# Optimization experiments

Hardware: AMD Instinct MI355X
Metric: run time of the kernel (lower is better)

## Reference

```python
import jax, jax.numpy as jnp
import numpy as np

B, S, H = 1, 2048, 1024          # batch, seq, hidden_size
INTER, K, DST, DTR = 2048, 4, 16, 64  # intermediate, kernel, ssm_state, dt_rank


def setup_inputs() -> dict:
    key = jax.random.key(0)
    ks = jax.random.split(key, 10)
    sc = 0.02
    return {
        "x": jax.random.normal(ks[0], (B, S, H), jnp.float32),
        "W_in": jax.random.normal(ks[1], (H, 2 * INTER), jnp.float32) * sc,
        "conv_w": jax.random.normal(ks[2], (K, 1, INTER), jnp.float32) * sc,
        "conv_b": jax.random.normal(ks[3], (INTER,), jnp.float32) * sc,
        "W_x": jax.random.normal(ks[4], (INTER, DTR + 2 * DST), jnp.float32) * sc,
        "W_dt": jax.random.normal(ks[5], (DTR, INTER), jnp.float32) * sc,
        "b_dt": jax.random.normal(ks[6], (INTER,), jnp.float32) * sc,
        "A_log": jax.random.normal(ks[7], (INTER, DST), jnp.float32) * sc,
        "D": jax.random.normal(ks[8], (INTER,), jnp.float32) * sc,
        "W_out": jax.random.normal(ks[9], (INTER, H), jnp.float32) * sc,
    }


def _ssm(dA, dBu, C):
    # dA, dBu: (b, s, h, d); C: (b, s, d) -> y: (b, s, h)
    xs = (jnp.moveaxis(dA, 1, 0), jnp.moveaxis(dBu, 1, 0), jnp.moveaxis(C, 1, 0))
    state0 = jnp.zeros(dA.shape[:1] + dA.shape[2:], dA.dtype)  # (b, h, d)

    def step(state, inp):
        Ai, dBui, Ci = inp  # (b,h,d), (b,h,d), (b,d)
        state = Ai * state + dBui
        y = jnp.einsum('bhd,bd->bh', state, Ci)
        return state, y

    _, ys = jax.lax.scan(step, state0, xs)  # ys: (s, b, h)
    return jnp.moveaxis(ys, 0, 1)


def reference(x, W_in, conv_w, conv_b, W_x, W_dt, b_dt, A_log, D, W_out):
    proj = x @ W_in                              # (b, s, 2*inter)
    raw, gate = jnp.split(proj, 2, axis=-1)      # each (b, s, inter)

    # causal depthwise conv over time, groups = inter
    conv = jax.lax.conv_general_dilated(
        raw, conv_w, window_strides=(1,), padding=[(K - 1, 0)],
        dimension_numbers=('NWC', 'WIO', 'NWC'), feature_group_count=INTER)
    h = jax.nn.silu(conv + conv_b)               # (b, s, inter)

    ssm_p = h @ W_x                              # (b, s, dtr + 2*d)
    ts, Bmat, C = jnp.split(ssm_p, [DTR, DTR + DST], axis=-1)
    dt = jax.nn.softplus(ts @ W_dt + b_dt)       # (b, s, inter)

    A = -jnp.exp(A_log)                          # (inter, d)
    dA = jnp.exp(dt[..., None] * A)              # (b, s, inter, d)
    dBu = dt[..., None] * Bmat[:, :, None, :] * h[..., None]  # (b, s, inter, d)

    y = _ssm(dA, dBu, C)                         # (b, s, inter)
    y = y + h * D
    y = y * jax.nn.silu(gate)
    return y @ W_out                             # (b, s, hidden)
```

## Files before the change

kernel.cpp:

```cpp
#include <hip/hip_runtime.h>
#include <math.h>

#define SEQ   2048
#define HID   1024
#define INTER 2048
#define DST   16
#define DTR   64
#define NP    96
#define NC    64
#define LCH   32
#define KS    16

typedef _Float16 f16;
typedef _Float16 f16x8 __attribute__((ext_vector_type(8)));
typedef _Float16 f16x4v __attribute__((ext_vector_type(4)));
typedef float f32x4 __attribute__((ext_vector_type(4)));

__device__ __forceinline__ float sigmoidf_(float x) { return 1.0f / (1.0f + expf(-x)); }
__device__ __forceinline__ float siluf_(float x)    { return x * sigmoidf_(x); }
__device__ __forceinline__ float softplusf_(float x){ return (x > 20.0f) ? x : log1pf(expf(x)); }

__device__ __forceinline__ void tile_transpose(const float* __restrict__ W,
                                               f16* __restrict__ Wt,
                                               int K, int N, int bx, int by, int tid)
{
    __shared__ float t[32][33];
    const int n0 = bx * 32, k0 = by * 32;
    const int j = tid & 31, i0 = tid >> 5;
#pragma unroll
    for (int r = 0; r < 4; ++r)
        t[i0 + r * 8][j] = W[(size_t)(k0 + i0 + r * 8) * N + n0 + j];
    __syncthreads();
#pragma unroll
    for (int r = 0; r < 4; ++r)
        Wt[(size_t)(n0 + i0 + r * 8) * K + k0 + j] = (f16)t[j][i0 + r * 8];
}

__global__ __launch_bounds__(256) void prep_all(const float* __restrict__ x,
                                                const float* __restrict__ W_in,
                                                const float* __restrict__ W_out,
                                                const float* __restrict__ W_x,
                                                const float* __restrict__ W_dt,
                                                f16* __restrict__ xh,
                                                f16* __restrict__ W_in_t,
                                                f16* __restrict__ W_out_t,
                                                f16* __restrict__ WxT,
                                                f16* __restrict__ WdtT)
{
    const int bid = blockIdx.x, tid = threadIdx.x;
    if (bid < 2048) {
        int i = (bid * 256 + tid) * 4;
        float4 v = *(const float4*)&x[i];
        f16x4v o;
        o.x = (f16)v.x; o.y = (f16)v.y; o.z = (f16)v.z; o.w = (f16)v.w;
        *(f16x4v*)&xh[i] = o;
    } else if (bid < 6144) {
        int t = bid - 2048;
        tile_transpose(W_in, W_in_t, HID, 4096, t & 127, t >> 7, tid);
    } else if (bid < 8192) {
        int t = bid - 6144;
        tile_transpose(W_out, W_out_t, INTER, HID, t & 31, t >> 5, tid);
    } else if (bid < 8384) {
        int t = bid - 8192;
        tile_transpose(W_x, WxT, INTER, NP, t % 3, t / 3, tid);
    } else {
        int t = bid - 8384;
        tile_transpose(W_dt, WdtT, DTR, INTER, t & 63, t >> 6, tid);
    }
}

template<int BM, int BN, int KK, typename OutT>
__global__ __launch_bounds__(256) void gemm_f16mfma(const f16* __restrict__ Ah,
                                                    const f16* __restrict__ Bt,
                                                    OutT* __restrict__ C,
                                                    int N)
{
    constexpr int BK = 64;
    __shared__ __align__(16) f16 As[BM * BK];
    __shared__ __align__(16) f16 Bs[BN * BK];

    const int tid = threadIdx.x;
    const int wid = tid >> 6, lane = tid & 63;
    const int wr = wid >> 1, wc = wid & 1;
    const int m0 = blockIdx.y * BM, n0 = blockIdx.x * BN;
    const int l15 = lane & 15, lhi = lane >> 4;

    constexpr int MR = BM / 32;
    constexpr int NR = BN / 32;

    f32x4 acc[MR][NR] = {};

    for (int k0 = 0; k0 < KK; k0 += BK) {
        constexpr int CA = BM * BK * 2 / 1024;
#pragma unroll
        for (int c0 = 0; c0 < CA; c0 += 4) {
            int c = c0 + wid;
            int e = c * 64 + lane;
            int row = e >> 3, seg = e & 7;
            __builtin_amdgcn_global_load_lds(
                (const __attribute__((address_space(1))) unsigned int*)
                    (Ah + (size_t)(m0 + row) * KK + k0 + seg * 8),
                (__attribute__((address_space(3))) unsigned int*)(As + c * 512),
                16, 0, 0);
        }
        constexpr int CB = BN * BK * 2 / 1024;
#pragma unroll
        for (int c0 = 0; c0 < CB; c0 += 4) {
            int c = c0 + wid;
            int e = c * 64 + lane;
            int row = e >> 3, seg = e & 7;
            __builtin_amdgcn_global_load_lds(
                (const __attribute__((address_space(1))) unsigned int*)
                    (Bt + (size_t)(n0 + row) * KK + k0 + seg * 8),
                (__attribute__((address_space(3))) unsigned int*)(Bs + c * 512),
                16, 0, 0);
        }
        __syncthreads();

#pragma unroll
        for (int kk = 0; kk < BK; kk += 32) {
            f16x8 af[MR], bf[NR];
#pragma unroll
            for (int i = 0; i < MR; ++i)
                af[i] = *(const f16x8*)&As[(wr * (BM / 2) + i * 16 + l15) * BK + kk + lhi * 8];
#pragma unroll
            for (int n = 0; n < NR; ++n)
                bf[n] = *(const f16x8*)&Bs[(wc * (BN / 2) + n * 16 + l15) * BK + kk + lhi * 8];
#pragma unroll
            for (int i = 0; i < MR; ++i)
#pragma unroll
                for (int n = 0; n < NR; ++n)
                    acc[i][n] = __builtin_amdgcn_mfma_f32_16x16x32_f16(af[i], bf[n], acc[i][n], 0, 0, 0);
        }
        __syncthreads();
    }

#pragma unroll
    for (int i = 0; i < MR; ++i)
#pragma unroll
        for (int n = 0; n < NR; ++n)
#pragma unroll
            for (int r = 0; r < 4; ++r)
                C[(size_t)(m0 + wr * (BM / 2) + i * 16 + lhi * 4 + r) * N
                  + n0 + wc * (BN / 2) + n * 16 + l15] = (OutT)acc[i][n][r];
}

__global__ __launch_bounds__(256) void hwx_mfma(const f16* __restrict__ hh,
                                                const f16* __restrict__ WxT,
                                                float* __restrict__ partials)
{
    constexpr int BM = 128, BN = 96, BK = 64;
    __shared__ __align__(16) f16 As[BM * BK];
    __shared__ __align__(16) f16 Bs[BN * BK];

    const int tid = threadIdx.x;
    const int wid = tid >> 6, lane = tid & 63;
    const int wr = wid >> 1, wc = wid & 1;
    const int m0 = blockIdx.x * BM;
    const int ks = blockIdx.y;
    const int l15 = lane & 15, lhi = lane >> 4;

    constexpr int MR = 4, NR = 3;
    f32x4 acc[MR][NR] = {};

    for (int k0 = ks * 128; k0 < ks * 128 + 128; k0 += BK) {
#pragma unroll
        for (int c0 = 0; c0 < 16; c0 += 4) {
            int c = c0 + wid;
            int e = c * 64 + lane;
            int row = e >> 3, seg = e & 7;
            __builtin_amdgcn_global_load_lds(
                (const __attribute__((address_space(1))) unsigned int*)
                    (hh + (size_t)(m0 + row) * INTER + k0 + seg * 8),
                (__attribute__((address_space(3))) unsigned int*)(As + c * 512),
                16, 0, 0);
        }
#pragma unroll
        for (int c0 = 0; c0 < 12; c0 += 4) {
            int c = c0 + wid;
            int e = c * 64 + lane;
            int row = e >> 3, seg = e & 7;
            __builtin_amdgcn_global_load_lds(
                (const __attribute__((address_space(1))) unsigned int*)
                    (WxT + (size_t)row * INTER + k0 + seg * 8),
                (__attribute__((address_space(3))) unsigned int*)(Bs + c * 512),
                16, 0, 0);
        }
        __syncthreads();

#pragma unroll
        for (int kk = 0; kk < BK; kk += 32) {
            f16x8 af[MR], bf[NR];
#pragma unroll
            for (int i = 0; i < MR; ++i)
                af[i] = *(const f16x8*)&As[(wr * 64 + i * 16 + l15) * BK + kk + lhi * 8];
#pragma unroll
            for (int n = 0; n < NR; ++n)
                bf[n] = *(const f16x8*)&Bs[(wc * 48 + n * 16 + l15) * BK + kk + lhi * 8];
#pragma unroll
            for (int i = 0; i < MR; ++i)
#pragma unroll
                for (int n = 0; n < NR; ++n)
                    acc[i][n] = __builtin_amdgcn_mfma_f32_16x16x32_f16(af[i], bf[n], acc[i][n], 0, 0, 0);
        }
        __syncthreads();
    }

    float* P = partials + (size_t)ks * (SEQ * NP);
#pragma unroll
    for (int i = 0; i < MR; ++i)
#pragma unroll
        for (int n = 0; n < NR; ++n)
#pragma unroll
            for (int r = 0; r < 4; ++r)
                P[(size_t)(m0 + wr * 64 + i * 16 + lhi * 4 + r) * NP
                  + wc * 48 + n * 16 + l15] = acc[i][n][r];
}

__global__ __launch_bounds__(256) void reduce_partials(const float* __restrict__ partials,
                                                       float* __restrict__ ssm_p,
                                                       f16* __restrict__ tsh)
{
    int i = blockIdx.x * 256 + threadIdx.x;
    if (i < SEQ * NP) {
        float a = 0.0f;
#pragma unroll
        for (int c = 0; c < KS; ++c) a += partials[(size_t)c * (SEQ * NP) + i];
        int j = i % NP;
        if (j < DTR) tsh[(size_t)(i / NP) * DTR + j] = (f16)a;
        else         ssm_p[i] = a;
    }
}

__global__ __launch_bounds__(256) void dt_mfma(const f16* __restrict__ tsh,
                                               const f16* __restrict__ WdtT,
                                               const float* __restrict__ bdt,
                                               f16* __restrict__ dtbh)
{
    constexpr int BM = 128, BN = 128, BK = 64;
    __shared__ __align__(16) f16 As[BM * BK];
    __shared__ __align__(16) f16 Bs[BN * BK];

    const int tid = threadIdx.x;
    const int wid = tid >> 6, lane = tid & 63;
    const int wr = wid >> 1, wc = wid & 1;
    const int m0 = blockIdx.y * BM, n0 = blockIdx.x * BN;
    const int l15 = lane & 15, lhi = lane >> 4;

    constexpr int MR = 4, NR = 4;
    f32x4 acc[MR][NR] = {};

#pragma unroll
    for (int c0 = 0; c0 < 16; c0 += 4) {
        int c = c0 + wid;
        int e = c * 64 + lane;
        int row = e >> 3, seg = e & 7;
        __builtin_amdgcn_global_load_lds(
            (const __attribute__((address_space(1))) unsigned int*)
                (tsh + (size_t)(m0 + row) * DTR + seg * 8),
            (__attribute__((address_space(3))) unsigned int*)(As + c * 512),
            16, 0, 0);
        __builtin_amdgcn_global_load_lds(
            (const __attribute__((address_space(1))) unsigned int*)
                (WdtT + (size_t)(n0 + row) * DTR + seg * 8),
            (__attribute__((address_space(3))) unsigned int*)(Bs + c * 512),
            16, 0, 0);
    }
    __syncthreads();

#pragma unroll
    for (int kk = 0; kk < 64; kk += 32) {
        f16x8 af[MR], bf[NR];
#pragma unroll
        for (int i = 0; i < MR; ++i)
            af[i] = *(const f16x8*)&As[(wr * 64 + i * 16 + l15) * BK + kk + lhi * 8];
#pragma unroll
        for (int n = 0; n < NR; ++n)
            bf[n] = *(const f16x8*)&Bs[(wc * 64 + n * 16 + l15) * BK + kk + lhi * 8];
#pragma unroll
        for (int i = 0; i < MR; ++i)
#pragma unroll
            for (int n = 0; n < NR; ++n)
                acc[i][n] = __builtin_amdgcn_mfma_f32_16x16x32_f16(af[i], bf[n], acc[i][n], 0, 0, 0);
    }

#pragma unroll
    for (int i = 0; i < MR; ++i)
#pragma unroll
        for (int n = 0; n < NR; ++n) {
            int col = n0 + wc * 64 + n * 16 + l15;
            float bv = bdt[col];
#pragma unroll
            for (int r = 0; r < 4; ++r)
                dtbh[(size_t)(m0 + wr * 64 + i * 16 + lhi * 4 + r) * INTER + col] =
                    (f16)softplusf_(acc[i][n][r] + bv);
        }
}

__global__ __launch_bounds__(256) void conv_silu(const f16* __restrict__ projh,
                                                 const float* __restrict__ cw,
                                                 const float* __restrict__ cb,
                                                 f16* __restrict__ hh)
{
    int idx = blockIdx.x * 256 + threadIdx.x;
    int c8 = (idx & (INTER / 8 - 1)) * 8;
    int s = idx >> 8;
    float acc[8];
#pragma unroll
    for (int j = 0; j < 8; ++j) acc[j] = cb[c8 + j];
#pragma unroll
    for (int k = 0; k < 4; ++k) {
        int sp = s + k - 3;
        if (sp >= 0) {
            f16x8 p = *(const f16x8*)&projh[(size_t)sp * (2 * INTER) + c8];
#pragma unroll
            for (int j = 0; j < 8; ++j)
                acc[j] = fmaf((float)p[j], cw[k * INTER + c8 + j], acc[j]);
        }
    }
    f16x8 o;
#pragma unroll
    for (int j = 0; j < 8; ++j) o[j] = (f16)siluf_(acc[j]);
    *(f16x8*)&hh[(size_t)idx * 8] = o;
}

__global__ __launch_bounds__(256) void ssm_pass1(const f16* __restrict__ dtbh,
                                                 const f16* __restrict__ hh,
                                                 const float* __restrict__ ssm_p,
                                                 const float* __restrict__ A_log,
                                                 float* __restrict__ Sbuf,
                                                 float* __restrict__ Pbuf)
{
    const int h = blockIdx.x * 256 + threadIdx.x;
    const int c = blockIdx.y;
    const int s0 = c * LCH;

    __shared__ float Bs[LCH][DST];
    for (int j = threadIdx.x; j < LCH * DST; j += 256) {
        int r = j >> 4, dd = j & 15;
        Bs[r][dd] = ssm_p[(size_t)(s0 + r) * NP + DTR + dd];
    }
    __syncthreads();

    float A[DST], st[DST], P[DST];
#pragma unroll
    for (int d = 0; d < DST; ++d) {
        A[d] = -__expf(A_log[(size_t)h * DST + d]);
        st[d] = 0.0f;
        P[d] = 1.0f;
    }

    for (int r = 0; r < LCH; ++r) {
        float dtv = (float)dtbh[(size_t)(s0 + r) * INTER + h];
        float hv  = (float)hh[(size_t)(s0 + r) * INTER + h];
        float dh = dtv * hv;
#pragma unroll
        for (int d = 0; d < DST; ++d) {
            float da = __expf(dtv * A[d]);
            st[d] = fmaf(da, st[d], dh * Bs[r][d]);
            P[d] *= da;
        }
    }

    size_t base = ((size_t)c * INTER + h) * DST;
#pragma unroll
    for (int d = 0; d < DST; d += 4) {
        *(float4*)&Sbuf[base + d] = make_float4(st[d], st[d+1], st[d+2], st[d+3]);
        *(float4*)&Pbuf[base + d] = make_float4(P[d], P[d+1], P[d+2], P[d+3]);
    }
}

__global__ __launch_bounds__(256) void ssm_pass2(const float* __restrict__ Sbuf,
                                                 const float* __restrict__ Pbuf,
                                                 float* __restrict__ Cin)
{
    int i = blockIdx.x * 256 + threadIdx.x;
    float carry = 0.0f;
    for (int c = 0; c < NC; ++c) {
        size_t idx = (size_t)c * (INTER * DST) + i;
        Cin[idx] = carry;
        carry = fmaf(Pbuf[idx], carry, Sbuf[idx]);
    }
}

__global__ __launch_bounds__(256) void ssm_pass3(const f16* __restrict__ dtbh,
                                                 const f16* __restrict__ hh,
                                                 const float* __restrict__ ssm_p,
                                                 const f16* __restrict__ projh,
                                                 const float* __restrict__ A_log,
                                                 const float* __restrict__ Dvec,
                                                 const float* __restrict__ Cin,
                                                 f16* __restrict__ yh)
{
    const int h = blockIdx.x * 256 + threadIdx.x;
    const int c = blockIdx.y;
    const int s0 = c * LCH;

    __shared__ float Bs[LCH][DST];
    __shared__ float Cs[LCH][DST];
    for (int j = threadIdx.x; j < LCH * DST; j += 256) {
        int r = j >> 4, dd = j & 15;
        Bs[r][dd] = ssm_p[(size_t)(s0 + r) * NP + DTR + dd];
        Cs[r][dd] = ssm_p[(size_t)(s0 + r) * NP + DTR + DST + dd];
    }
    __syncthreads();

    float A[DST], st[DST];
    size_t base = ((size_t)c * INTER + h) * DST;
#pragma unroll
    for (int d = 0; d < DST; ++d) {
        A[d] = -__expf(A_log[(size_t)h * DST + d]);
        st[d] = Cin[base + d];
    }
    const float Dv = Dvec[h];

    for (int r = 0; r < LCH; ++r) {
        float dtv = (float)dtbh[(size_t)(s0 + r) * INTER + h];
        float hv  = (float)hh[(size_t)(s0 + r) * INTER + h];
        float g   = (float)projh[(size_t)(s0 + r) * (2 * INTER) + INTER + h];
        float dh = dtv * hv;
        float y = 0.0f;
#pragma unroll
        for (int d = 0; d < DST; ++d) {
            float da = __expf(dtv * A[d]);
            st[d] = fmaf(da, st[d], dh * Bs[r][d]);
            y = fmaf(st[d], Cs[r][d], y);
        }
        y = fmaf(hv, Dv, y);
        yh[(size_t)(s0 + r) * INTER + h] = (f16)(y * siluf_(g));
    }
}

extern "C" void kernel_launch(void* const* d_in, const int* in_sizes, int n_in,
                              void* d_out, int out_size, void* d_ws, size_t ws_size,
                              hipStream_t stream)
{
    const float* x      = (const float*)d_in[0];
    const float* W_in   = (const float*)d_in[1];
    const float* conv_w = (const float*)d_in[2];
    const float* conv_b = (const float*)d_in[3];
    const float* W_x    = (const float*)d_in[4];
    const float* W_dt   = (const float*)d_in[5];
    const float* b_dt   = (const float*)d_in[6];
    const float* A_log  = (const float*)d_in[7];
    const float* Dv     = (const float*)d_in[8];
    const float* W_out  = (const float*)d_in[9];
    float* out = (float*)d_out;

    float* ws = (float*)d_ws;
    f16*  projh  = (f16*)ws;
    f16*  hh     = (f16*)(ws + 4194304);
    f16*  dtbh   = (f16*)(ws + 6291456);
    f16*  yh     = (f16*)(ws + 8388608);
    f16*  xh     = (f16*)(ws + 10485760);
    f16*  W_in_t = (f16*)(ws + 11534336);
    f16*  W_out_t= (f16*)(ws + 13631488);
    f16*  WxT    = (f16*)(ws + 14680064);
    f16*  tsh    = (f16*)(ws + 14778368);
    f16*  WdtT   = (f16*)(ws + 14843904);
    float* ssm_p = ws + 14909440;
    float* parts = ws + 15106048;
    float* Sbuf  = ws + 18251776;
    float* Pbuf  = ws + 20348928;
    float* Cin   = ws + 22446080;

    prep_all<<<8512, 256, 0, stream>>>(x, W_in, W_out, W_x, W_dt,
                                       xh, W_in_t, W_out_t, WxT, WdtT);

    gemm_f16mfma<128, 128, HID, f16><<<dim3(4096 / 128, SEQ / 128), 256, 0, stream>>>(
        xh, W_in_t, projh, 2 * INTER);

    conv_silu<<<(SEQ * INTER / 8) / 256, 256, 0, stream>>>(projh, conv_w, conv_b, hh);

    hwx_mfma<<<dim3(SEQ / 128, KS), 256, 0, stream>>>(hh, WxT, parts);
    reduce_partials<<<(SEQ * NP + 255) / 256, 256, 0, stream>>>(parts, ssm_p, tsh);

    dt_mfma<<<dim3(INTER / 128, SEQ / 128), 256, 0, stream>>>(tsh, WdtT, b_dt, dtbh);

    ssm_pass1<<<dim3(INTER / 256, NC), 256, 0, stream>>>(dtbh, hh, ssm_p, A_log, Sbuf, Pbuf);
    ssm_pass2<<<(INTER * DST) / 256, 256, 0, stream>>>(Sbuf, Pbuf, Cin);
    ssm_pass3<<<dim3(INTER / 256, NC), 256, 0, stream>>>(dtbh, hh, ssm_p, projh, A_log, Dv, Cin, yh);

    gemm_f16mfma<64, 128, INTER, float><<<dim3(HID / 128, SEQ / 64), 256, 0, stream>>>(
        yh, W_out_t, out, HID);
}
```

Baseline: 184.0 us.

## Add XCD-aware tile swizzle to GEMMs, store split-K partials in fp16, vectorize reduce

Flattens the 2D grids of the GEMM, hwx and dt kernels into 1D and remaps block IDs so that consecutive tiles land on the same XCD, aiming for better L2 reuse of shared operand tiles. The split-K partials of h@W_x are now stored as fp16 instead of fp32, which halves that buffer's traffic. The reduction kernel reads 8 halfs per thread with vector loads and writes vectorized outputs. Loop unrolling is added to ssm_pass2. The fp16 partials lose precision in the ts/B/C projections, which feed the dt and SSM recurrence.

```diff
diff --git a/kernel.cpp b/kernel.cpp
--- a/kernel.cpp
+++ b/kernel.cpp
@@ -19,6 +19,12 @@
 __device__ __forceinline__ float sigmoidf_(float x) { return 1.0f / (1.0f + expf(-x)); }
 __device__ __forceinline__ float siluf_(float x)    { return x * sigmoidf_(x); }
 __device__ __forceinline__ float softplusf_(float x){ return (x > 20.0f) ? x : log1pf(expf(x)); }
+
+__device__ __forceinline__ int xcd_swz(int bid, int nwg)
+{
+    int cpx = nwg >> 3;
+    return (bid & 7) * cpx + (bid >> 3);
+}
 
 __device__ __forceinline__ void tile_transpose(const float* __restrict__ W,
                                                f16* __restrict__ Wt,
@@ -73,16 +79,19 @@
 __global__ __launch_bounds__(256) void gemm_f16mfma(const f16* __restrict__ Ah,
                                                     const f16* __restrict__ Bt,
                                                     OutT* __restrict__ C,
-                                                    int N)
+                                                    int N, int nbx)
 {
     constexpr int BK = 64;
     __shared__ __align__(16) f16 As[BM * BK];
     __shared__ __align__(16) f16 Bs[BN * BK];
 
+    const int tile = xcd_swz(blockIdx.x, gridDim.x);
+    const int bx = tile % nbx, by = tile / nbx;
+
     const int tid = threadIdx.x;
     const int wid = tid >> 6, lane = tid & 63;
     const int wr = wid >> 1, wc = wid & 1;
-    const int m0 = blockIdx.y * BM, n0 = blockIdx.x * BN;
+    const int m0 = by * BM, n0 = bx * BN;
     const int l15 = lane & 15, lhi = lane >> 4;
 
     constexpr int MR = BM / 32;
@@ -147,17 +156,19 @@
 
 __global__ __launch_bounds__(256) void hwx_mfma(const f16* __restrict__ hh,
                                                 const f16* __restrict__ WxT,
-                                                float* __restrict__ partials)
+                                                f16* __restrict__ partials)
 {
     constexpr int BM = 128, BN = 96, BK = 64;
     __shared__ __align__(16) f16 As[BM * BK];
     __shared__ __align__(16) f16 Bs[BN * BK];
 
+    const int tile = xcd_swz(blockIdx.x, gridDim.x);
+    const int bxm = tile & 15, ks = tile >> 4;
+
     const int tid = threadIdx.x;
     const int wid = tid >> 6, lane = tid & 63;
     const int wr = wid >> 1, wc = wid & 1;
-    const int m0 = blockIdx.x * BM;
-    const int ks = blockIdx.y;
+    const int m0 = bxm * BM;
     const int l15 = lane & 15, lhi = lane >> 4;
 
     constexpr int MR = 4, NR = 3;
@@ -206,7 +217,7 @@
         __syncthreads();
     }
 
-    float* P = partials + (size_t)ks * (SEQ * NP);
+    f16* P = partials + (size_t)ks * (SEQ * NP);
 #pragma unroll
     for (int i = 0; i < MR; ++i)
 #pragma unroll
@@ -214,21 +225,31 @@
 #pragma unroll
             for (int r = 0; r < 4; ++r)
                 P[(size_t)(m0 + wr * 64 + i * 16 + lhi * 4 + r) * NP
-                  + wc * 48 + n * 16 + l15] = acc[i][n][r];
-}
-
-__global__ __launch_bounds__(256) void reduce_partials(const float* __restrict__ partials,
+                  + wc * 48 + n * 16 + l15] = (f16)acc[i][n][r];
+}
+
+__global__ __launch_bounds__(256) void reduce_partials(const f16* __restrict__ partials,
                                                        float* __restrict__ ssm_p,
                                                        f16* __restrict__ tsh)
 {
-    int i = blockIdx.x * 256 + threadIdx.x;
-    if (i < SEQ * NP) {
-        float a = 0.0f;
-#pragma unroll
-        for (int c = 0; c < KS; ++c) a += partials[(size_t)c * (SEQ * NP) + i];
-        int j = i % NP;
-        if (j < DTR) tsh[(size_t)(i / NP) * DTR + j] = (f16)a;
-        else         ssm_p[i] = a;
+    int t = blockIdx.x * 256 + threadIdx.x;
+    int i8 = t * 8;
+    int s = i8 / NP, j0 = i8 % NP;
+    float a[8] = {};
+#pragma unroll
+    for (int c = 0; c < KS; ++c) {
+        f16x8 v = *(const f16x8*)&partials[(size_t)c * (SEQ * NP) + i8];
+#pragma unroll
+        for (int j = 0; j < 8; ++j) a[j] += (float)v[j];
+    }
+    if (j0 < DTR) {
+        f16x8 o;
+#pragma unroll
+        for (int j = 0; j < 8; ++j) o[j] = (f16)a[j];
+        *(f16x8*)&tsh[(size_t)s * DTR + j0] = o;
+    } else {
+        *(float4*)&ssm_p[(size_t)s * NP + j0]     = make_float4(a[0], a[1], a[2], a[3]);
+        *(float4*)&ssm_p[(size_t)s * NP + j0 + 4] = make_float4(a[4], a[5], a[6], a[7]);
     }
 }
 
@@ -241,10 +262,13 @@
     __shared__ __align__(16) f16 As[BM * BK];
     __shared__ __align__(16) f16 Bs[BN * BK];
 
+    const int tile = xcd_swz(blockIdx.x, gridDim.x);
+    const int bx = tile & 15, by = tile >> 4;
+
     const int tid = threadIdx.x;
     const int wid = tid >> 6, lane = tid & 63;
     const int wr = wid >> 1, wc = wid & 1;
-    const int m0 = blockIdx.y * BM, n0 = blockIdx.x * BN;
+    const int m0 = by * BM, n0 = bx * BN;
     const int l15 = lane & 15, lhi = lane >> 4;
 
     constexpr int MR = 4, NR = 4;
@@ -376,6 +400,7 @@
 {
     int i = blockIdx.x * 256 + threadIdx.x;
     float carry = 0.0f;
+#pragma unroll 4
     for (int c = 0; c < NC; ++c) {
         size_t idx = (size_t)c * (INTER * DST) + i;
         Cin[idx] = carry;
@@ -459,28 +484,28 @@
     f16*  tsh    = (f16*)(ws + 14778368);
     f16*  WdtT   = (f16*)(ws + 14843904);
     float* ssm_p = ws + 14909440;
-    float* parts = ws + 15106048;
-    float* Sbuf  = ws + 18251776;
-    float* Pbuf  = ws + 20348928;
-    float* Cin   = ws + 22446080;
+    f16*  parts  = (f16*)(ws + 15106048);
+    float* Sbuf  = ws + 16678912;
+    float* Pbuf  = ws + 18776064;
+    float* Cin   = ws + 20873216;
 
     prep_all<<<8512, 256, 0, stream>>>(x, W_in, W_out, W_x, W_dt,
                                        xh, W_in_t, W_out_t, WxT, WdtT);
 
-    gemm_f16mfma<128, 128, HID, f16><<<dim3(4096 / 128, SEQ / 128), 256, 0, stream>>>(
-        xh, W_in_t, projh, 2 * INTER);
+    gemm_f16mfma<128, 128, HID, f16><<<512, 256, 0, stream>>>(
+        xh, W_in_t, projh, 2 * INTER, 32);
 
     conv_silu<<<(SEQ * INTER / 8) / 256, 256, 0, stream>>>(projh, conv_w, conv_b, hh);
 
-    hwx_mfma<<<dim3(SEQ / 128, KS), 256, 0, stream>>>(hh, WxT, parts);
-    reduce_partials<<<(SEQ * NP + 255) / 256, 256, 0, stream>>>(parts, ssm_p, tsh);
-
-    dt_mfma<<<dim3(INTER / 128, SEQ / 128), 256, 0, stream>>>(tsh, WdtT, b_dt, dtbh);
+    hwx_mfma<<<256, 256, 0, stream>>>(hh, WxT, parts);
+    reduce_partials<<<(SEQ * NP / 8) / 256, 256, 0, stream>>>(parts, ssm_p, tsh);
+
+    dt_mfma<<<256, 256, 0, stream>>>(tsh, WdtT, b_dt, dtbh);
 
     ssm_pass1<<<dim3(INTER / 256, NC), 256, 0, stream>>>(dtbh, hh, ssm_p, A_log, Sbuf, Pbuf);
     ssm_pass2<<<(INTER * DST) / 256, 256, 0, stream>>>(Sbuf, Pbuf, Cin);
     ssm_pass3<<<dim3(INTER / 256, NC), 256, 0, stream>>>(dtbh, hh, ssm_p, projh, A_log, Dv, Cin, yh);
 
-    gemm_f16mfma<64, 128, INTER, float><<<dim3(HID / 128, SEQ / 64), 256, 0, stream>>>(
-        yh, W_out_t, out, HID);
-}
+    gemm_f16mfma<64, 128, INTER, float><<<256, 256, 0, stream>>>(
+        yh, W_out_t, out, HID, 8);
+}
```

After: 185.1 us. Within noise of the previous version (+0.6%).
